# Optimization experiments

Hardware: AMD Instinct MI355X
Metric: run time of the kernel (lower is better)

## Reference

```python
import jax, jax.numpy as jnp
import numpy as np

N = 2097152
N_LAYERS = 32
N_SUB = 8


def setup_inputs() -> dict:
    key = jax.random.key(0)
    k1, k2, k3, k4 = jax.random.split(key, 4)
    return {
        "x": jax.random.normal(k1, (N, 2), dtype=jnp.float32),
        "act_w": 0.05 * jax.random.normal(k2, (N_LAYERS,), dtype=jnp.float32),
        "bias_b": 0.05 * jax.random.normal(k3, (N_LAYERS, 2), dtype=jnp.float32),
        "lin_w": 0.05 * jax.random.normal(k4, (N_LAYERS, N_SUB), dtype=jnp.float32),
    }


def _forward_chain(q, p, act_w, bias_b, lin_w):
    # Apply Modules[0..end] with inverse=0.
    n_layers, n_sub = lin_w.shape
    for i in range(n_layers):
        # activation module: up adds w*tanh(p) to q, low adds w*tanh(q) to p
        if i % 2 == 0:
            q = q + act_w[i] * jnp.tanh(p)
        else:
            p = p + act_w[i] * jnp.tanh(q)
        # bias module (inserted at j == 0)
        q = q + bias_b[i, 0]
        p = p + bias_b[i, 1]
        # linear shear modules
        for j in range(n_sub):
            if j % 2 == 0:   # linear_module_up: q += w*p
                q = q + lin_w[i, j] * p
            else:            # linear_module_low: p += w*q
                p = p + lin_w[i, j] * q
    return q, p


def _inverse_chain(q, p, act_w, bias_b, lin_w):
    # Apply all modules in reverse order with inverse=1 (negated weights).
    n_layers, n_sub = lin_w.shape
    for i in reversed(range(n_layers)):
        for j in reversed(range(n_sub)):
            if j % 2 == 0:
                q = q - lin_w[i, j] * p
            else:
                p = p - lin_w[i, j] * q
        q = q - bias_b[i, 0]
        p = p - bias_b[i, 1]
        if i % 2 == 0:
            q = q - act_w[i] * jnp.tanh(p)
        else:
            p = p - act_w[i] * jnp.tanh(q)
    return q, p


def reference(x, act_w, bias_b, lin_w):
    q, p = x[..., 0], x[..., 1]
    q, p = _forward_chain(q, p, act_w, bias_b, lin_w)
    # time reversal: multiply by [1, -1]
    p = -p
    q, p = _inverse_chain(q, p, act_w, bias_b, lin_w)
    # final module-0 inverse is included in _inverse_chain; scale by [1, -1]
    return jnp.stack([q, -p], axis=-1)
```

## Files before the change

kernel.cpp:

```cpp
#include <hip/hip_runtime.h>

constexpr int NL = 32;
constexpr int PPT = 8;

__device__ __forceinline__ float tanh_poly(float x) {
#if __has_builtin(__builtin_amdgcn_fmed3f)
    float t = __builtin_amdgcn_fmed3f(x, -3.4f, 3.4f);
#else
    float t = fminf(fmaxf(x, -3.4f), 3.4f);
#endif
    float s = t * t;
    float u = fmaf(s, 2.3524e-06f, -1.000059e-04f);
    u = fmaf(s, u, 1.7302740e-03f);
    u = fmaf(s, u, -1.5874717e-02f);
    u = fmaf(s, u, 8.5976700e-02f);
    u = fmaf(s, u, -3.0595090e-01f);
    u = fmaf(s, u, 9.9691910e-01f);
    return t * u;
}

__global__ void build_tables(const float* __restrict__ act_w,
                             const float* __restrict__ bias_b,
                             const float* __restrict__ lin_w,
                             float* __restrict__ tab)
{
    int t = threadIdx.x;
    if (t >= NL) return;
    float m00 = 1.f, m01 = 0.f, m10 = 0.f, m11 = 1.f;
    #pragma unroll
    for (int j = 0; j < 8; ++j) {
        float w = lin_w[t * 8 + j];
        if ((j & 1) == 0) { m00 = fmaf(w, m10, m00); m01 = fmaf(w, m11, m01); }
        else              { m10 = fmaf(w, m00, m10); m11 = fmaf(w, m01, m11); }
    }
    float b0 = bias_b[2 * t], b1 = bias_b[2 * t + 1];
    float aw = act_w[t];
    float* f = &tab[t * 16];
    f[0] = m00; f[1] = m01; f[2] = m10; f[3] = m11;
    f[4] = fmaf(m00, b0, m01 * b1);
    f[5] = fmaf(m10, b0, m11 * b1);
    f[6] = aw; f[7] = 0.f;
    f[8]  = m11; f[9]  = -m01; f[10] = -m10; f[11] = m00;
    f[12] = -b0; f[13] = -b1; f[14] = -aw; f[15] = 0.f;
}

__global__ __launch_bounds__(256) void sympnet_main(
    const float* __restrict__ x,
    const float* __restrict__ tab,
    float* __restrict__ out)
{
    int gid = blockIdx.x * blockDim.x + threadIdx.x;
    const float4* x4 = (const float4*)x;
    float4* out4 = (float4*)out;
    long base = (long)gid * (PPT / 2);

    float Q[PPT], P[PPT];
    #pragma unroll
    for (int k = 0; k < PPT / 2; ++k) {
        float4 v = x4[base + k];
        Q[2*k]   = v.x; P[2*k]   = v.y;
        Q[2*k+1] = v.z; P[2*k+1] = v.w;
    }

    #pragma unroll 1
    for (int i = 0; i < NL; i += 2) {
        const float* f = &tab[i * 16];
        float m00=f[0], m01=f[1], m10=f[2], m11=f[3], C0=f[4], C1=f[5], T=f[6];
        const float* g = &tab[(i + 1) * 16];
        float n00=g[0], n01=g[1], n10=g[2], n11=g[3], E0=g[4], E1=g[5], U=g[6];
        #pragma unroll
        for (int k = 0; k < PPT; ++k) {
            float Qa = fmaf(T, tanh_poly(P[k]), Q[k]);
            float Qn = fmaf(m00, Qa, fmaf(m01, P[k], C0));
            float Pn = fmaf(m10, Qa, fmaf(m11, P[k], C1));
            float Pa = fmaf(U, tanh_poly(Qn), Pn);
            Q[k] = fmaf(n00, Qn, fmaf(n01, Pa, E0));
            P[k] = fmaf(n10, Qn, fmaf(n11, Pa, E1));
        }
    }

    #pragma unroll
    for (int k = 0; k < PPT; ++k) P[k] = -P[k];

    #pragma unroll 1
    for (int i = NL - 1; i > 0; i -= 2) {
        const float* g = &tab[i * 16 + 8];
        float n00=g[0], n01=g[1], n10=g[2], n11=g[3], E0=g[4], E1=g[5], U=g[6];
        const float* f = &tab[(i - 1) * 16 + 8];
        float m00=f[0], m01=f[1], m10=f[2], m11=f[3], C0=f[4], C1=f[5], T=f[6];
        #pragma unroll
        for (int k = 0; k < PPT; ++k) {
            float Qn = fmaf(n00, Q[k], fmaf(n01, P[k], E0));
            float Pn = fmaf(n10, Q[k], fmaf(n11, P[k], E1));
            Pn = fmaf(U, tanh_poly(Qn), Pn);
            float Q2 = fmaf(m00, Qn, fmaf(m01, Pn, C0));
            float P2 = fmaf(m10, Qn, fmaf(m11, Pn, C1));
            Q[k] = fmaf(T, tanh_poly(P2), Q2);
            P[k] = P2;
        }
    }

    #pragma unroll
    for (int k = 0; k < PPT / 2; ++k) {
        float4 o;
        o.x = Q[2*k];   o.y = -P[2*k];
        o.z = Q[2*k+1]; o.w = -P[2*k+1];
        out4[base + k] = o;
    }
}

extern "C" void kernel_launch(void* const* d_in, const int* in_sizes, int n_in,
                              void* d_out, int out_size, void* d_ws, size_t ws_size,
                              hipStream_t stream) {
    const float* x      = (const float*)d_in[0];
    const float* act_w  = (const float*)d_in[1];
    const float* bias_b = (const float*)d_in[2];
    const float* lin_w  = (const float*)d_in[3];
    float* out = (float*)d_out;
    float* tab = (float*)d_ws;

    build_tables<<<1, 64, 0, stream>>>(act_w, bias_b, lin_w, tab);

    int npts = in_sizes[0] / 2;
    int nthreads = npts / PPT;
    int blocks = (nthreads + 255) / 256;
    sympnet_main<<<blocks, 256, 0, stream>>>(x, tab, out);
}
```

Baseline: 105.8 us.

## Fuse table build into main kernel, use LDS tables and strided float2 I/O

Removes the separate table-building launch: every block computes the 32 per-layer folded matrices itself and keeps them in shared memory as float4s. The time-reversal negation of P is folded into the last inverse layer's matrix. Points are now assigned with a grid stride of nthreads, using float2 accesses that coalesce across the wavefront. It also adds launch_bounds occupancy hints, at the cost of redundant per-block table work and a __syncthreads.

```diff
diff --git a/kernel.cpp b/kernel.cpp
--- a/kernel.cpp
+++ b/kernel.cpp
@@ -19,93 +19,82 @@
     return t * u;
 }
 
-__global__ void build_tables(const float* __restrict__ act_w,
-                             const float* __restrict__ bias_b,
-                             const float* __restrict__ lin_w,
-                             float* __restrict__ tab)
+__global__ __launch_bounds__(256, 4) void sympnet_main(
+    const float* __restrict__ x,
+    const float* __restrict__ act_w,
+    const float* __restrict__ bias_b,
+    const float* __restrict__ lin_w,
+    float* __restrict__ out,
+    int nthreads)
 {
+    __shared__ float4 tf[NL][2];
+    __shared__ float4 ti[NL][2];
+
     int t = threadIdx.x;
-    if (t >= NL) return;
-    float m00 = 1.f, m01 = 0.f, m10 = 0.f, m11 = 1.f;
-    #pragma unroll
-    for (int j = 0; j < 8; ++j) {
-        float w = lin_w[t * 8 + j];
-        if ((j & 1) == 0) { m00 = fmaf(w, m10, m00); m01 = fmaf(w, m11, m01); }
-        else              { m10 = fmaf(w, m00, m10); m11 = fmaf(w, m01, m11); }
+    if (t < NL) {
+        float m00 = 1.f, m01 = 0.f, m10 = 0.f, m11 = 1.f;
+        #pragma unroll
+        for (int j = 0; j < 8; ++j) {
+            float w = lin_w[t * 8 + j];
+            if ((j & 1) == 0) { m00 = fmaf(w, m10, m00); m01 = fmaf(w, m11, m01); }
+            else              { m10 = fmaf(w, m00, m10); m11 = fmaf(w, m01, m11); }
+        }
+        float b0 = bias_b[2 * t], b1 = bias_b[2 * t + 1], aw = act_w[t];
+        tf[t][0] = make_float4(m00, m01, m10, m11);
+        tf[t][1] = make_float4(fmaf(m00, b0, m01 * b1), fmaf(m10, b0, m11 * b1), aw, 0.f);
+        float s = (t == NL - 1) ? -1.f : 1.f;
+        ti[t][0] = make_float4(m11, s * (-m01), -m10, s * m00);
+        ti[t][1] = make_float4(-b0, -b1, -aw, 0.f);
     }
-    float b0 = bias_b[2 * t], b1 = bias_b[2 * t + 1];
-    float aw = act_w[t];
-    float* f = &tab[t * 16];
-    f[0] = m00; f[1] = m01; f[2] = m10; f[3] = m11;
-    f[4] = fmaf(m00, b0, m01 * b1);
-    f[5] = fmaf(m10, b0, m11 * b1);
-    f[6] = aw; f[7] = 0.f;
-    f[8]  = m11; f[9]  = -m01; f[10] = -m10; f[11] = m00;
-    f[12] = -b0; f[13] = -b1; f[14] = -aw; f[15] = 0.f;
-}
+    __syncthreads();
 
-__global__ __launch_bounds__(256) void sympnet_main(
-    const float* __restrict__ x,
-    const float* __restrict__ tab,
-    float* __restrict__ out)
-{
-    int gid = blockIdx.x * blockDim.x + threadIdx.x;
-    const float4* x4 = (const float4*)x;
-    float4* out4 = (float4*)out;
-    long base = (long)gid * (PPT / 2);
+    int gid = blockIdx.x * blockDim.x + t;
+    const float2* x2 = (const float2*)x;
+    float2* o2 = (float2*)out;
 
     float Q[PPT], P[PPT];
     #pragma unroll
-    for (int k = 0; k < PPT / 2; ++k) {
-        float4 v = x4[base + k];
-        Q[2*k]   = v.x; P[2*k]   = v.y;
-        Q[2*k+1] = v.z; P[2*k+1] = v.w;
+    for (int k = 0; k < PPT; ++k) {
+        float2 v = x2[gid + k * nthreads];
+        Q[k] = v.x; P[k] = v.y;
     }
 
     #pragma unroll 1
     for (int i = 0; i < NL; i += 2) {
-        const float* f = &tab[i * 16];
-        float m00=f[0], m01=f[1], m10=f[2], m11=f[3], C0=f[4], C1=f[5], T=f[6];
-        const float* g = &tab[(i + 1) * 16];
-        float n00=g[0], n01=g[1], n10=g[2], n11=g[3], E0=g[4], E1=g[5], U=g[6];
+        float4 Fm = tf[i][0],     Fc = tf[i][1];
+        float4 Gm = tf[i + 1][0], Gc = tf[i + 1][1];
         #pragma unroll
         for (int k = 0; k < PPT; ++k) {
-            float Qa = fmaf(T, tanh_poly(P[k]), Q[k]);
-            float Qn = fmaf(m00, Qa, fmaf(m01, P[k], C0));
-            float Pn = fmaf(m10, Qa, fmaf(m11, P[k], C1));
-            float Pa = fmaf(U, tanh_poly(Qn), Pn);
-            Q[k] = fmaf(n00, Qn, fmaf(n01, Pa, E0));
-            P[k] = fmaf(n10, Qn, fmaf(n11, Pa, E1));
+            float Qa = fmaf(Fc.z, tanh_poly(P[k]), Q[k]);
+            float Qn = fmaf(Fm.x, Qa, fmaf(Fm.y, P[k], Fc.x));
+            float Pn = fmaf(Fm.z, Qa, fmaf(Fm.w, P[k], Fc.y));
+            float Pa = fmaf(Gc.z, tanh_poly(Qn), Pn);
+            Q[k] = fmaf(Gm.x, Qn, fmaf(Gm.y, Pa, Gc.x));
+            P[k] = fmaf(Gm.z, Qn, fmaf(Gm.w, Pa, Gc.y));
         }
     }
 
-    #pragma unroll
-    for (int k = 0; k < PPT; ++k) P[k] = -P[k];
 
     #pragma unroll 1
     for (int i = NL - 1; i > 0; i -= 2) {
-        const float* g = &tab[i * 16 + 8];
-        float n00=g[0], n01=g[1], n10=g[2], n11=g[3], E0=g[4], E1=g[5], U=g[6];
-        const float* f = &tab[(i - 1) * 16 + 8];
-        float m00=f[0], m01=f[1], m10=f[2], m11=f[3], C0=f[4], C1=f[5], T=f[6];
+        float4 Gm = ti[i][0],     Gc = ti[i][1];
+        float4 Fm = ti[i - 1][0], Fc = ti[i - 1][1];
         #pragma unroll
         for (int k = 0; k < PPT; ++k) {
-            float Qn = fmaf(n00, Q[k], fmaf(n01, P[k], E0));
-            float Pn = fmaf(n10, Q[k], fmaf(n11, P[k], E1));
-            Pn = fmaf(U, tanh_poly(Qn), Pn);
-            float Q2 = fmaf(m00, Qn, fmaf(m01, Pn, C0));
-            float P2 = fmaf(m10, Qn, fmaf(m11, Pn, C1));
-            Q[k] = fmaf(T, tanh_poly(P2), Q2);
+            float Qn = fmaf(Gm.x, Q[k], fmaf(Gm.y, P[k], Gc.x));
+            float Pn = fmaf(Gm.z, Q[k], fmaf(Gm.w, P[k], Gc.y));
+            Pn = fmaf(Gc.z, tanh_poly(Qn), Pn);
+            float Q2 = fmaf(Fm.x, Qn, fmaf(Fm.y, Pn, Fc.x));
+            float P2 = fmaf(Fm.z, Qn, fmaf(Fm.w, Pn, Fc.y));
+            Q[k] = fmaf(Fc.z, tanh_poly(P2), Q2);
             P[k] = P2;
         }
     }
 
     #pragma unroll
-    for (int k = 0; k < PPT / 2; ++k) {
-        float4 o;
-        o.x = Q[2*k];   o.y = -P[2*k];
-        o.z = Q[2*k+1]; o.w = -P[2*k+1];
-        out4[base + k] = o;
+    for (int k = 0; k < PPT; ++k) {
+        float2 o; o.x = Q[k]; o.y = -P[k];
+        o2[gid + k * nthreads] = o;
     }
 }
 
@@ -117,12 +106,9 @@
     const float* bias_b = (const float*)d_in[2];
     const float* lin_w  = (const float*)d_in[3];
     float* out = (float*)d_out;
-    float* tab = (float*)d_ws;
-
-    build_tables<<<1, 64, 0, stream>>>(act_w, bias_b, lin_w, tab);
 
     int npts = in_sizes[0] / 2;
     int nthreads = npts / PPT;
-    int blocks = (nthreads + 255) / 256;
-    sympnet_main<<<blocks, 256, 0, stream>>>(x, tab, out);
+    int blocks = nthreads / 256;
+    sympnet_main<<<blocks, 256, 0, stream>>>(x, act_w, bias_b, lin_w, out, nthreads);
 }
```

New measurement: 106.9 us. About the same (+1.0%).
